# Performance work log

Measured on AMD Instinct MI355X. Metric: run time of the kernel, lower is better.

## Reference

```python
import jax, jax.numpy as jnp
import numpy as np

N_NODES = 50000
N_EDGES = 1200000
NODE_DIM = 64
HIDDEN = 64
OUT_DIM = 1
N_LAYERS = 3


def setup_inputs() -> dict:
    key = jax.random.key(0)
    ks = jax.random.split(key, 16)
    inp = {
        "H": jax.random.normal(ks[0], (N_NODES, NODE_DIM), dtype=jnp.float32),
        "edge_index": jax.random.randint(ks[1], (2, N_EDGES), 0, N_NODES, dtype=jnp.int64),
        "E": jax.random.normal(ks[2], (N_EDGES, 16), dtype=jnp.float32),
    }
    # per-layer params: node_encoder (enc) and update_w (upd); weights stored [in, out]
    for i in range(N_LAYERS):
        in_dim = NODE_DIM if i == 0 else HIDDEN
        s = 1.0 / np.sqrt(in_dim)
        inp[f"enc_w{i}"] = jax.random.uniform(ks[3 + 2 * i], (in_dim, HIDDEN), jnp.float32, -s, s)
        inp[f"enc_b{i}"] = jax.random.uniform(ks[4 + 2 * i], (HIDDEN,), jnp.float32, -s, s)
        sh = 1.0 / np.sqrt(HIDDEN)
        inp[f"upd_w{i}"] = jax.random.uniform(ks[9 + 2 * i], (HIDDEN, HIDDEN), jnp.float32, -sh, sh)
        inp[f"upd_b{i}"] = jax.random.uniform(ks[10 + 2 * i], (HIDDEN,), jnp.float32, -sh, sh)
    so = 1.0 / np.sqrt(HIDDEN)
    inp["out_w"] = jax.random.uniform(ks[15], (HIDDEN, OUT_DIM), jnp.float32, -so, so)
    inp["out_b"] = jnp.zeros((OUT_DIM,), jnp.float32)
    return inp


def _gcn_forward(H, edge_index, params):
    u, v = edge_index[0], edge_index[1]
    # symmetric normalization with implicit self-loop degree bump (calc_norm_factor)
    deg = jax.ops.segment_sum(jnp.ones(u.shape[0], H.dtype), u, num_segments=N_NODES) + 1.0
    dis = deg ** -0.5  # deg >= 1, never inf
    norm = dis[u] * dis[v]  # [n_edges]
    for i in range(N_LAYERS):
        enc_w, enc_b, upd_w, upd_b = params[i]
        H = H @ enc_w + enc_b                      # node_encoder
        msgs = norm[:, None] * H[u]                # gather + scale
        agg = jax.ops.segment_sum(msgs, v, num_segments=N_NODES)  # scatter-add
        H = jax.nn.relu((agg + H) @ upd_w + upd_b)  # update + ReLU (dropout = identity in eval)
    return H


def reference(H, edge_index, E, enc_w0, enc_b0, upd_w0, upd_b0, enc_w1, enc_b1,
              upd_w1, upd_b1, enc_w2, enc_b2, upd_w2, upd_b2, out_w, out_b):
    params = [(enc_w0, enc_b0, upd_w0, upd_b0),
              (enc_w1, enc_b1, upd_w1, upd_b1),
              (enc_w2, enc_b2, upd_w2, upd_b2)]
    Hf = _gcn_forward(H, edge_index, params)
    graph_emb = jnp.mean(Hf, axis=0, keepdims=True)  # [1, HIDDEN] readout (batch=None)
    return graph_emb @ out_w + out_b                 # [1, OUT_DIM]
```

## Files before the change

kernel.cpp:

```cpp
#include <hip/hip_runtime.h>
#include <hip/hip_fp16.h>

#define NN 50000
#define NE 1200000
#define DIM 64
#define NB 782
#define SLICES 512
#define ES 2344
#define VCAP 2048
#define GB 782
#define FRONT_LDS 33792
#define FB 3125

__device__ __forceinline__ void fold_body(char* smem, int i,
                                          const float* __restrict__ E,
                                          const float* __restrict__ e,
                                          const float* __restrict__ U,
                                          const float* __restrict__ ub,
                                          float* __restrict__ Wp,
                                          float* __restrict__ cvec,
                                          float* __restrict__ dvec) {
    float (*Es)[64] = (float(*)[64])smem;
    float (*Us)[64] = (float(*)[64])(smem + 16384);
    int t = threadIdx.x;
#pragma unroll
    for (int j = 0; j < 4; ++j) {
        int idx = t + j * 256;
        int r = idx >> 4, c = (idx & 15) << 2;
        *(float4*)&Es[r][c] = *(const float4*)&E[r * 64 + c];
        *(float4*)&Us[r][c] = *(const float4*)&U[r * 64 + c];
    }
    __syncthreads();
    int r0 = (t >> 4) * 4;
    int c0 = (t & 15) * 4;
    float acc[4][4] = {};
#pragma unroll
    for (int k = 0; k < 64; k += 4) {
        float4 b0 = *(float4*)&Us[k + 0][c0];
        float4 b1 = *(float4*)&Us[k + 1][c0];
        float4 b2 = *(float4*)&Us[k + 2][c0];
        float4 b3 = *(float4*)&Us[k + 3][c0];
#pragma unroll
        for (int q = 0; q < 4; ++q) {
            float4 av = *(float4*)&Es[r0 + q][k];
            acc[q][0] = fmaf(av.x, b0.x, fmaf(av.y, b1.x, fmaf(av.z, b2.x, fmaf(av.w, b3.x, acc[q][0]))));
            acc[q][1] = fmaf(av.x, b0.y, fmaf(av.y, b1.y, fmaf(av.z, b2.y, fmaf(av.w, b3.y, acc[q][1]))));
            acc[q][2] = fmaf(av.x, b0.z, fmaf(av.y, b1.z, fmaf(av.z, b2.z, fmaf(av.w, b3.z, acc[q][2]))));
            acc[q][3] = fmaf(av.x, b0.w, fmaf(av.y, b1.w, fmaf(av.z, b2.w, fmaf(av.w, b3.w, acc[q][3]))));
        }
    }
    float* W = Wp + i * 4096;
#pragma unroll
    for (int q = 0; q < 4; ++q)
        *(float4*)&W[(r0 + q) * 64 + c0] = make_float4(acc[q][0], acc[q][1], acc[q][2], acc[q][3]);
    if (t < 64) {
        float sc = 0.f;
        for (int k = 0; k < 64; ++k) sc = fmaf(e[k], Us[k][t], sc);
        cvec[i * 64 + t] = sc;
        dvec[i * 64 + t] = sc + ub[t];
    }
}


__device__ __forceinline__ void lsort_body(char* smem, const int* __restrict__ ei,
                                           ushort* __restrict__ usort,
                                           int* __restrict__ ebuf,
                                           int* __restrict__ lpart_u,
                                           int* __restrict__ lpart_v,
                                           int s) {
    int* hist = (int*)smem;
    int* wsum = (int*)(smem + 3136);
    ushort* sbu = (ushort*)(smem + 4160);
    int* sbv = (int*)(smem + 8848);
    int t = threadIdx.x;
    int w = t >> 6, l = t & 63;
    int e0 = s * ES, e1 = min(e0 + ES, NE), len = e1 - e0;
    int i0 = t * 4;

    int uv[10], vv[10];
#pragma unroll
    for (int j = 0; j < 10; ++j) {
        int e = e0 + t + j * 256;
        uv[j] = (e < e1) ? ei[e] : -1;
        vv[j] = (e < e1) ? ei[NE + e] : -1;
    }

    for (int i = t; i < NB; i += 256) hist[i] = 0;
    __syncthreads();
#pragma unroll
    for (int j = 0; j < 10; ++j)
        if (uv[j] >= 0) atomicAdd(&hist[uv[j] >> 6], 1);
    __syncthreads();
    {
        int h0 = (i0 + 0 < NB) ? hist[i0 + 0] : 0;
        int h1 = (i0 + 1 < NB) ? hist[i0 + 1] : 0;
        int h2 = (i0 + 2 < NB) ? hist[i0 + 2] : 0;
        int h3 = (i0 + 3 < NB) ? hist[i0 + 3] : 0;
        int p1 = h0, p2 = h0 + h1, p3 = p2 + h2, p4 = p3 + h3;
        int inc = p4;
        for (int o = 1; o < 64; o <<= 1) {
            int x = __shfl_up(inc, o, 64);
            if (l >= o) inc += x;
        }
        if (l == 63) wsum[w] = inc;
        __syncthreads();
        int base = 0;
#pragma unroll
        for (int j = 0; j < 4; ++j) if (j < w) base += wsum[j];
        int total = wsum[0] + wsum[1] + wsum[2] + wsum[3];
        int excl = base + inc - p4;
        int* lpu = lpart_u + s * (NB + 1);
        if (i0 + 0 < NB) { lpu[i0 + 0] = excl;      hist[i0 + 0] = excl; }
        if (i0 + 1 < NB) { lpu[i0 + 1] = excl + p1; hist[i0 + 1] = excl + p1; }
        if (i0 + 2 < NB) { lpu[i0 + 2] = excl + p2; hist[i0 + 2] = excl + p2; }
        if (i0 + 3 < NB) { lpu[i0 + 3] = excl + p3; hist[i0 + 3] = excl + p3; }
        if (t == 255) lpu[NB] = total;
    }
    __syncthreads();
#pragma unroll
    for (int j = 0; j < 10; ++j)
        if (uv[j] >= 0) {
            int pos = atomicAdd(&hist[uv[j] >> 6], 1);
            sbu[pos] = (ushort)uv[j];
        }
    __syncthreads();
    for (int i = t; i < len; i += 256) usort[e0 + i] = sbu[i];
    for (int i = t; i < NB; i += 256) hist[i] = 0;
    __syncthreads();

#pragma unroll
    for (int j = 0; j < 10; ++j)
        if (vv[j] >= 0) atomicAdd(&hist[vv[j] >> 6], 1);
    __syncthreads();
    {
        int h0 = (i0 + 0 < NB) ? hist[i0 + 0] : 0;
        int h1 = (i0 + 1 < NB) ? hist[i0 + 1] : 0;
        int h2 = (i0 + 2 < NB) ? hist[i0 + 2] : 0;
        int h3 = (i0 + 3 < NB) ? hist[i0 + 3] : 0;
        int p1 = h0, p2 = h0 + h1, p3 = p2 + h2, p4 = p3 + h3;
        int inc = p4;
        for (int o = 1; o < 64; o <<= 1) {
            int x = __shfl_up(inc, o, 64);
            if (l >= o) inc += x;
        }
        if (l == 63) wsum[w] = inc;
        __syncthreads();
        int base = 0;
#pragma unroll
        for (int j = 0; j < 4; ++j) if (j < w) base += wsum[j];
        int total = wsum[0] + wsum[1] + wsum[2] + wsum[3];
        int excl = base + inc - p4;
        int* lpv = lpart_v + s * (NB + 1);
        if (i0 + 0 < NB) { lpv[i0 + 0] = excl;      hist[i0 + 0] = excl; }
        if (i0 + 1 < NB) { lpv[i0 + 1] = excl + p1; hist[i0 + 1] = excl + p1; }
        if (i0 + 2 < NB) { lpv[i0 + 2] = excl + p2; hist[i0 + 2] = excl + p2; }
        if (i0 + 3 < NB) { lpv[i0 + 3] = excl + p3; hist[i0 + 3] = excl + p3; }
        if (t == 255) lpv[NB] = total;
    }
    __syncthreads();
#pragma unroll
    for (int j = 0; j < 10; ++j)
        if (vv[j] >= 0) {
            int pos = atomicAdd(&hist[vv[j] >> 6], 1);
            sbv[pos] = uv[j] | ((vv[j] & 63) << 16);
        }
    __syncthreads();
    for (int i = t; i < len; i += 256) ebuf[e0 + i] = sbv[i];
}

__device__ __forceinline__ void gemm0_body(char* smem, int blk,
                                           const float* __restrict__ H,
                                           const float* __restrict__ E0,
                                           const float* __restrict__ U0,
                                           __half* __restrict__ Ph) {
    float (*As)[68] = (float(*)[68])smem;
    float (*Bs)[64] = (float(*)[64])(smem + 17408);
    int t = threadIdx.x;
    int row0 = blk * 64;
#pragma unroll
    for (int i = 0; i < 4; ++i) {
        int idx = t + i * 256;
        int r = idx >> 4, c = (idx & 15) << 2;
        float4 val = make_float4(0.f, 0.f, 0.f, 0.f);
        if (row0 + r < NN) val = *(const float4*)&H[(size_t)(row0 + r) * DIM + c];
        *(float4*)&As[r][c] = val;
        *(float4*)&Bs[r][c] = *(const float4*)&E0[r * DIM + c];
    }
    __syncthreads();
    int r0 = (t >> 4) * 4;
    int c0 = (t & 15) * 4;
    float acc[4][4] = {};
#pragma unroll
    for (int k = 0; k < 64; k += 4) {
        float4 b0 = *(float4*)&Bs[k + 0][c0];
        float4 b1 = *(float4*)&Bs[k + 1][c0];
        float4 b2 = *(float4*)&Bs[k + 2][c0];
        float4 b3 = *(float4*)&Bs[k + 3][c0];
#pragma unroll
        for (int i = 0; i < 4; ++i) {
            float4 av = *(float4*)&As[r0 + i][k];
            acc[i][0] = fmaf(av.x, b0.x, fmaf(av.y, b1.x, fmaf(av.z, b2.x, fmaf(av.w, b3.x, acc[i][0]))));
            acc[i][1] = fmaf(av.x, b0.y, fmaf(av.y, b1.y, fmaf(av.z, b2.y, fmaf(av.w, b3.y, acc[i][1]))));
            acc[i][2] = fmaf(av.x, b0.z, fmaf(av.y, b1.z, fmaf(av.z, b2.z, fmaf(av.w, b3.z, acc[i][2]))));
            acc[i][3] = fmaf(av.x, b0.w, fmaf(av.y, b1.w, fmaf(av.z, b2.w, fmaf(av.w, b3.w, acc[i][3]))));
        }
    }
    __syncthreads();
#pragma unroll
    for (int i = 0; i < 4; ++i)
        *(float4*)&As[r0 + i][c0] = make_float4(acc[i][0], acc[i][1], acc[i][2], acc[i][3]);
#pragma unroll
    for (int i = 0; i < 4; ++i) {
        int idx = t + i * 256;
        int r = idx >> 4, c = (idx & 15) << 2;
        *(float4*)&Bs[r][c] = *(const float4*)&U0[r * DIM + c];
    }
    __syncthreads();
    float acc2[4][4] = {};
#pragma unroll
    for (int k = 0; k < 64; k += 4) {
        float4 b0 = *(float4*)&Bs[k + 0][c0];
        float4 b1 = *(float4*)&Bs[k + 1][c0];
        float4 b2 = *(float4*)&Bs[k + 2][c0];
        float4 b3 = *(float4*)&Bs[k + 3][c0];
#pragma unroll
        for (int i = 0; i < 4; ++i) {
            float4 av = *(float4*)&As[r0 + i][k];
            acc2[i][0] = fmaf(av.x, b0.x, fmaf(av.y, b1.x, fmaf(av.z, b2.x, fmaf(av.w, b3.x, acc2[i][0]))));
            acc2[i][1] = fmaf(av.x, b0.y, fmaf(av.y, b1.y, fmaf(av.z, b2.y, fmaf(av.w, b3.y, acc2[i][1]))));
            acc2[i][2] = fmaf(av.x, b0.z, fmaf(av.y, b1.z, fmaf(av.z, b2.z, fmaf(av.w, b3.z, acc2[i][2]))));
            acc2[i][3] = fmaf(av.x, b0.w, fmaf(av.y, b1.w, fmaf(av.z, b2.w, fmaf(av.w, b3.w, acc2[i][3]))));
        }
    }
#pragma unroll
    for (int i = 0; i < 4; ++i) {
        int r = row0 + r0 + i;
        if (r < NN) {
            __half2 p0 = __floats2half2_rn(acc2[i][0], acc2[i][1]);
            __half2 p1 = __floats2half2_rn(acc2[i][2], acc2[i][3]);
            uint2 pk;
            pk.x = *(unsigned int*)&p0;
            pk.y = *(unsigned int*)&p1;
            *(uint2*)&Ph[(size_t)r * DIM + c0] = pk;
        }
    }
}

__global__ __launch_bounds__(256, 2) void k_front(const int* __restrict__ ei,
                                                  ushort* __restrict__ usort,
                                                  int* __restrict__ ebuf,
                                                  int* __restrict__ lpart_u,
                                                  int* __restrict__ lpart_v,
                                                  const float* __restrict__ H,
                                                  const float* __restrict__ E0, const float* __restrict__ e0,
                                                  const float* __restrict__ U0, const float* __restrict__ ub0,
                                                  const float* __restrict__ E1, const float* __restrict__ e1,
                                                  const float* __restrict__ U1, const float* __restrict__ ub1,
                                                  const float* __restrict__ E2, const float* __restrict__ e2,
                                                  const float* __restrict__ U2, const float* __restrict__ ub2,
                                                  __half* __restrict__ Ph,
                                                  float* __restrict__ Wp,
                                                  float* __restrict__ cvec,
                                                  float* __restrict__ dvec) {
    extern __shared__ char smem[];
    int b = blockIdx.x;
    if (b < 256)
        lsort_body(smem, ei, usort, ebuf, lpart_u, lpart_v, b);
    else if (b < 512)
        gemm0_body(smem, b - 256, H, E0, U0, Ph);
    else if (b < 768)
        lsort_body(smem, ei, usort, ebuf, lpart_u, lpart_v, b - 256);
    else if (b < 512 + GB)
        gemm0_body(smem, b - 512, H, E0, U0, Ph);
    else {
        int i = b - (512 + GB);
        const float* E  = (i == 0) ? E0  : (i == 1) ? E1  : E2;
        const float* e  = (i == 0) ? e0  : (i == 1) ? e1  : e2;
        const float* U  = (i == 0) ? U0  : (i == 1) ? U1  : U2;
        const float* ub = (i == 0) ? ub0 : (i == 1) ? ub1 : ub2;
        fold_body(smem, i, E, e, U, ub, Wp, cvec, dvec);
    }
}

__global__ __launch_bounds__(256) void k_prep(const ushort* __restrict__ usort,
                                              const int* __restrict__ lpart_u,
                                              const int* __restrict__ ebuf,
                                              const int* __restrict__ lpart_v,
                                              float* __restrict__ dis,
                                              ushort* __restrict__ edges,
                                              int* __restrict__ row_ptr,
                                              float* __restrict__ colsum) {
    __shared__ int cache[VCAP];
    __shared__ int cnt[64];
    __shared__ int cur[64];
    __shared__ int wsum4[4];
    __shared__ int rsum4[4];
    __shared__ int sh[64];
    int bid = blockIdx.x;
    int t = threadIdx.x, w = t >> 6, l = t & 63;
    if (bid < NB) {
        int b = bid;
        if (b == 0 && t < 64) colsum[t] = 0.f;
        if (t < 64) sh[t] = 0;
        __syncthreads();
        for (int s = t; s < SLICES; s += 256) {
            const int* row = lpart_u + s * (NB + 1);
            int st = row[b], en = row[b + 1];
            for (int i = st; i < en; ++i)
                atomicAdd(&sh[usort[s * ES + i] & 63], 1);
        }
        __syncthreads();
        int n = (b << 6) + t;
        if (t < 64 && n < NN) dis[n] = rsqrtf((float)sh[t] + 1.0f);
        return;
    }
    int b = bid - NB;
    int s0 = t * 2, s1 = t * 2 + 1;
    const int* r0p = lpart_v + s0 * (NB + 1);
    const int* r1p = lpart_v + s1 * (NB + 1);
    int a0 = r0p[b], a1 = r0p[b + 1];
    int c0 = r1p[b], c1 = r1p[b + 1];
    int len0 = a1 - a0, len1 = c1 - c0;
    int tl = len0 + len1;
    int ts = a0 + c0;
    int inc = tl;
    for (int o = 1; o < 64; o <<= 1) {
        int x = __shfl_up(inc, o, 64);
        if (l >= o) inc += x;
    }
    int tss = ts;
    for (int off = 32; off; off >>= 1) tss += __shfl_down(tss, off, 64);
    if (l == 63) wsum4[w] = inc;
    if (l == 0) rsum4[w] = tss;
    if (t < 64) cnt[t] = 0;
    __syncthreads();
    int base = 0;
#pragma unroll
    for (int j = 0; j < 4; ++j) if (j < w) base += wsum4[j];
    int n = wsum4[0] + wsum4[1] + wsum4[2] + wsum4[3];
    int rbase = rsum4[0] + rsum4[1] + rsum4[2] + rsum4[3];
    int pos = base + inc - tl;
    if (n <= VCAP) {
        for (int i = 0; i < len0; ++i) cache[pos + i] = ebuf[s0 * ES + a0 + i];
        int pos1 = pos + len0;
        for (int i = 0; i < len1; ++i) cache[pos1 + i] = ebuf[s1 * ES + c0 + i];
        __syncthreads();
        for (int i = t; i < n; i += 256)
            atomicAdd(&cnt[(cache[i] >> 16) & 63], 1);
        __syncthreads();
        if (w == 0) {
            int c = cnt[l];
            int inc2 = c;
            for (int o = 1; o < 64; o <<= 1) {
                int x = __shfl_up(inc2, o, 64);
                if (l >= o) inc2 += x;
            }
            int excl = inc2 - c;
            cur[l] = rbase + excl;
            row_ptr[(b << 6) + l] = rbase + excl;
        }
        __syncthreads();
        for (int i = t; i < n; i += 256) {
            int rec = cache[i];
            int p2 = atomicAdd(&cur[(rec >> 16) & 63], 1);
            edges[p2] = (ushort)(rec & 0xFFFF);
        }
    } else {
        for (int s = t; s < SLICES; s += 256) {
            const int* row = lpart_v + s * (NB + 1);
            int st = row[b], en = row[b + 1];
            for (int i = st; i < en; ++i)
                atomicAdd(&cnt[(ebuf[s * ES + i] >> 16) & 63], 1);
        }
        __syncthreads();
        if (w == 0) {
            int c = cnt[l];
            int inc2 = c;
            for (int o = 1; o < 64; o <<= 1) {
                int x = __shfl_up(inc2, o, 64);
                if (l >= o) inc2 += x;
            }
            int excl = inc2 - c;
            cur[l] = rbase + excl;
            row_ptr[(b << 6) + l] = rbase + excl;
        }
        __syncthreads();
        for (int s = t; s < SLICES; s += 256) {
            const int* row = lpart_v + s * (NB + 1);
            int st = row[b], en = row[b + 1];
            for (int i = st; i < en; ++i) {
                int rec = ebuf[s * ES + i];
                int p2 = atomicAdd(&cur[(rec >> 16) & 63], 1);
                edges[p2] = (ushort)(rec & 0xFFFF);
            }
        }
    }
}

template<bool FIRST>
__device__ __forceinline__ void agg_node(const uint4* __restrict__ Pq4,
                                         const float* __restrict__ dis,
                                         const int* __restrict__ row_ptr,
                                         const ushort* __restrict__ edges,
                                         const float* __restrict__ cvec,
                                         const float* __restrict__ dvec,
                                         float* __restrict__ sarr,
                                         ushort* se, float* swt,
                                         int node, int l, int g, int p,
                                         float out[8]) {
    int start = row_ptr[node];
    int num = row_ptr[node + 1] - start;
    float4 a0 = {0.f, 0.f, 0.f, 0.f};
    float4 a1 = {0.f, 0.f, 0.f, 0.f};
    float sw = 0.f;
    for (int base = 0; base < num; base += 64) {
        int lim = min(64, num - base);
        ushort u = 0;
        float wv = 0.f;
        if (l < lim) { u = edges[start + base + l]; wv = dis[u]; }
        se[l] = u;
        swt[l] = wv;
        __builtin_amdgcn_wave_barrier();
        int octs = (lim + 7) >> 3;
        int rr[8]; float ww[8]; uint4 hh[8];
#pragma unroll
        for (int q = 0; q < 8; ++q)
            if (q < octs) { rr[q] = se[8 * q + g]; ww[q] = swt[8 * q + g]; }
#pragma unroll
        for (int q = 0; q < 8; ++q)
            if (q < octs) hh[q] = Pq4[(rr[q] << 3) + p];
#pragma unroll
        for (int q = 0; q < 8; ++q)
            if (q < octs) {
                float wt = ww[q];
                if (FIRST) sw += wt;
                float2 f0 = __half22float2(*(const __half2*)&hh[q].x);
                float2 f1 = __half22float2(*(const __half2*)&hh[q].y);
                float2 f2 = __half22float2(*(const __half2*)&hh[q].z);
                float2 f3 = __half22float2(*(const __half2*)&hh[q].w);
                a0.x = fmaf(wt, f0.x, a0.x);
                a0.y = fmaf(wt, f0.y, a0.y);
                a0.z = fmaf(wt, f1.x, a0.z);
                a0.w = fmaf(wt, f1.y, a0.w);
                a1.x = fmaf(wt, f2.x, a1.x);
                a1.y = fmaf(wt, f2.y, a1.y);
                a1.z = fmaf(wt, f3.x, a1.z);
                a1.w = fmaf(wt, f3.y, a1.w);
            }
        __builtin_amdgcn_wave_barrier();
    }
#pragma unroll
    for (int m = 8; m < 64; m <<= 1) {
        a0.x += __shfl_xor(a0.x, m, 64);
        a0.y += __shfl_xor(a0.y, m, 64);
        a0.z += __shfl_xor(a0.z, m, 64);
        a0.w += __shfl_xor(a0.w, m, 64);
        a1.x += __shfl_xor(a1.x, m, 64);
        a1.y += __shfl_xor(a1.y, m, 64);
        a1.z += __shfl_xor(a1.z, m, 64);
        a1.w += __shfl_xor(a1.w, m, 64);
        if (FIRST) sw += __shfl_xor(sw, m, 64);
    }
    if (g == 0) {
        float dv = dis[node];
        float sv;
        if (FIRST) {
            sv = dv * sw;
            if (p == 0) sarr[node] = sv;
        } else {
            sv = sarr[node];
        }
        uint4 pv = Pq4[(node << 3) + p];
        float2 s0 = __half22float2(*(const __half2*)&pv.x);
        float2 s1 = __half22float2(*(const __half2*)&pv.y);
        float2 s2 = __half22float2(*(const __half2*)&pv.z);
        float2 s3 = __half22float2(*(const __half2*)&pv.w);
        float4 cA = *(const float4*)&cvec[p << 3];
        float4 cB = *(const float4*)&cvec[(p << 3) + 4];
        float4 dA = *(const float4*)&dvec[p << 3];
        float4 dB = *(const float4*)&dvec[(p << 3) + 4];
        out[0] = fmaxf(fmaf(dv, a0.x, s0.x) + fmaf(sv, cA.x, dA.x), 0.f);
        out[1] = fmaxf(fmaf(dv, a0.y, s0.y) + fmaf(sv, cA.y, dA.y), 0.f);
        out[2] = fmaxf(fmaf(dv, a0.z, s1.x) + fmaf(sv, cA.z, dA.z), 0.f);
        out[3] = fmaxf(fmaf(dv, a0.w, s1.y) + fmaf(sv, cA.w, dA.w), 0.f);
        out[4] = fmaxf(fmaf(dv, a1.x, s2.x) + fmaf(sv, cB.x, dB.x), 0.f);
        out[5] = fmaxf(fmaf(dv, a1.y, s2.y) + fmaf(sv, cB.y, dB.y), 0.f);
        out[6] = fmaxf(fmaf(dv, a1.z, s3.x) + fmaf(sv, cB.z, dB.z), 0.f);
        out[7] = fmaxf(fmaf(dv, a1.w, s3.y) + fmaf(sv, cB.w, dB.w), 0.f);
    }
}

template<bool FIRST>
__global__ __launch_bounds__(256) void k_agggemm(const uint4* __restrict__ Pq4,
                                                 const float* __restrict__ dis,
                                                 const int* __restrict__ row_ptr,
                                                 const ushort* __restrict__ edges,
                                                 const float* __restrict__ cvec,
                                                 const float* __restrict__ dvec,
                                                 float* __restrict__ sarr,
                                                 const float* __restrict__ W,
                                                 __half* __restrict__ Phout) {
    __shared__ float As[16][68];
    __shared__ float Bs[64][64];
    __shared__ ushort se[4][64];
    __shared__ float swt[4][64];
    int t = threadIdx.x, w = t >> 6, l = t & 63;
    int g = l >> 3, p = l & 7;
    int node0 = blockIdx.x << 4;
#pragma unroll
    for (int i = 0; i < 4; ++i) {
        int idx = t + i * 256;
        int r = idx >> 4, c = (idx & 15) << 2;
        *(float4*)&Bs[r][c] = *(const float4*)&W[r * 64 + c];
    }
#pragma unroll 1
    for (int nn = 0; nn < 4; ++nn) {
        int node = node0 + (w << 2) + nn;
        float out[8];
        agg_node<FIRST>(Pq4, dis, row_ptr, edges, cvec, dvec, sarr,
                        se[w], swt[w], node, l, g, p, out);
        if (g == 0) {
            int r = (w << 2) + nn;
            *(float4*)&As[r][p << 3] = make_float4(out[0], out[1], out[2], out[3]);
            *(float4*)&As[r][(p << 3) + 4] = make_float4(out[4], out[5], out[6], out[7]);
        }
    }
    __syncthreads();
    int r = t >> 4;
    int c0 = (t & 15) << 2;
    float acc0 = 0.f, acc1 = 0.f, acc2 = 0.f, acc3 = 0.f;
#pragma unroll
    for (int k = 0; k < 64; k += 4) {
        float4 b0 = *(float4*)&Bs[k + 0][c0];
        float4 b1 = *(float4*)&Bs[k + 1][c0];
        float4 b2 = *(float4*)&Bs[k + 2][c0];
        float4 b3 = *(float4*)&Bs[k + 3][c0];
        float4 av = *(float4*)&As[r][k];
        acc0 = fmaf(av.x, b0.x, fmaf(av.y, b1.x, fmaf(av.z, b2.x, fmaf(av.w, b3.x, acc0))));
        acc1 = fmaf(av.x, b0.y, fmaf(av.y, b1.y, fmaf(av.z, b2.y, fmaf(av.w, b3.y, acc1))));
        acc2 = fmaf(av.x, b0.z, fmaf(av.y, b1.z, fmaf(av.z, b2.z, fmaf(av.w, b3.z, acc2))));
        acc3 = fmaf(av.x, b0.w, fmaf(av.y, b1.w, fmaf(av.z, b2.w, fmaf(av.w, b3.w, acc3))));
    }
    __half2 h0 = __floats2half2_rn(acc0, acc1);
    __half2 h1 = __floats2half2_rn(acc2, acc3);
    uint2 pk;
    pk.x = *(unsigned int*)&h0;
    pk.y = *(unsigned int*)&h1;
    *(uint2*)&Phout[(size_t)(node0 + r) * DIM + c0] = pk;
}

__global__ __launch_bounds__(256) void k_agg3(const uint4* __restrict__ Pq4,
                                              const float* __restrict__ dis,
                                              const int* __restrict__ row_ptr,
                                              const ushort* __restrict__ edges,
                                              const float* __restrict__ cvec,
                                              const float* __restrict__ dvec,
                                              float* __restrict__ sarr,
                                              __half* __restrict__ Hh) {
    __shared__ ushort se[4][64];
    __shared__ float swt[4][64];
    int t = threadIdx.x, w = t >> 6, l = t & 63;
    int g = l >> 3, p = l & 7;
    int node = (blockIdx.x << 2) + w;
    float out[8];
    agg_node<false>(Pq4, dis, row_ptr, edges, cvec, dvec, sarr,
                    se[w], swt[w], node, l, g, p, out);
    if (g == 0) {
        __half2 h0 = __floats2half2_rn(out[0], out[1]);
        __half2 h1 = __floats2half2_rn(out[2], out[3]);
        __half2 h2 = __floats2half2_rn(out[4], out[5]);
        __half2 h3 = __floats2half2_rn(out[6], out[7]);
        uint4 pk;
        pk.x = *(unsigned int*)&h0;
        pk.y = *(unsigned int*)&h1;
        pk.z = *(unsigned int*)&h2;
        pk.w = *(unsigned int*)&h3;
        *(uint4*)&Hh[((size_t)node << 6) + (p << 3)] = pk;
    }
}

__global__ __launch_bounds__(256) void k_colsum(const __half* __restrict__ Hh,
                                                float* __restrict__ colsum) {
    __shared__ float scs[64];
    int t = threadIdx.x;
    if (t < 64) scs[t] = 0.f;
    __syncthreads();
    int p = t & 7;
    float a[8] = {};
    for (int r = blockIdx.x * 32 + (t >> 3); r < NN; r += 256 * 32) {
        uint4 hv = *(const uint4*)&Hh[((size_t)r << 6) + (p << 3)];
        float2 f0 = __half22float2(*(const __half2*)&hv.x);
        float2 f1 = __half22float2(*(const __half2*)&hv.y);
        float2 f2 = __half22float2(*(const __half2*)&hv.z);
        float2 f3 = __half22float2(*(const __half2*)&hv.w);
        a[0] += f0.x; a[1] += f0.y; a[2] += f1.x; a[3] += f1.y;
        a[4] += f2.x; a[5] += f2.y; a[6] += f3.x; a[7] += f3.y;
    }
#pragma unroll
    for (int j = 0; j < 8; ++j) atomicAdd(&scs[(p << 3) + j], a[j]);
    __syncthreads();
    if (t < 64) atomicAdd(&colsum[t], scs[t]);
}

__global__ void k_out(const float* __restrict__ colsum, const float* __restrict__ out_w,
                      const float* __restrict__ out_b, float* __restrict__ out) {
    int f = threadIdx.x;
    float v = colsum[f] * (1.0f / (float)NN) * out_w[f];
    for (int off = 32; off; off >>= 1) v += __shfl_down(v, off, 64);
    if (f == 0) out[0] = v + out_b[0];
}

extern "C" void kernel_launch(void* const* d_in, const int* in_sizes, int n_in,
                              void* d_out, int out_size, void* d_ws, size_t ws_size,
                              hipStream_t stream) {
    const float* H  = (const float*)d_in[0];
    const int*   ei = (const int*)d_in[1];
    const float* enc_w[3] = { (const float*)d_in[3], (const float*)d_in[7],  (const float*)d_in[11] };
    const float* enc_b[3] = { (const float*)d_in[4], (const float*)d_in[8],  (const float*)d_in[12] };
    const float* upd_w[3] = { (const float*)d_in[5], (const float*)d_in[9],  (const float*)d_in[13] };
    const float* upd_b[3] = { (const float*)d_in[6], (const float*)d_in[10], (const float*)d_in[14] };
    const float* out_w = (const float*)d_in[15];
    const float* out_b = (const float*)d_in[16];
    float* out = (float*)d_out;

    size_t off = 0;
    auto carve = [&](size_t bytes) {
        void* p = (char*)d_ws + off;
        off = (off + bytes + 255) & ~(size_t)255;
        return p;
    };
    int*    lpart_u = (int*)carve((size_t)SLICES * (NB + 1) * 4);
    int*    lpart_v = (int*)carve((size_t)SLICES * (NB + 1) * 4);
    float*  dis     = (float*)carve((size_t)NN * 4);
    float*  sarr    = (float*)carve((size_t)NN * 4);
    ushort* usort   = (ushort*)carve((size_t)SLICES * ES * 2);
    int*    ebuf    = (int*)carve((size_t)SLICES * ES * 4);
    ushort* edges   = (ushort*)carve((size_t)NE * 2);
    int*    row_ptr = (int*)carve((size_t)(NN + 65) * 4);
    __half* PhA     = (__half*)carve((size_t)NN * DIM * 2);
    __half* PhB     = (__half*)carve((size_t)NN * DIM * 2);
    __half* Hh      = (__half*)carve((size_t)NN * DIM * 2);
    float*  Wp      = (float*)carve(3 * 64 * 64 * 4);
    float*  cvec    = (float*)carve(3 * 64 * 4);
    float*  dvec    = (float*)carve(3 * 64 * 4);
    float*  colsum  = (float*)carve(64 * 4);

    const uint4* PqA = (const uint4*)PhA;
    const uint4* PqB = (const uint4*)PhB;

    k_front<<<512 + GB + 3, 256, FRONT_LDS, stream>>>(ei, usort, ebuf, lpart_u, lpart_v, H,
                                                      enc_w[0], enc_b[0], upd_w[0], upd_b[0],
                                                      enc_w[1], enc_b[1], upd_w[1], upd_b[1],
                                                      enc_w[2], enc_b[2], upd_w[2], upd_b[2],
                                                      PhA, Wp, cvec, dvec);
    k_prep<<<2 * NB, 256, 0, stream>>>(usort, lpart_u, ebuf, lpart_v,
                                       dis, edges, row_ptr, colsum);

    k_agggemm<true><<<FB, 256, 0, stream>>>(PqA, dis, row_ptr, edges,
                                            cvec + 0, dvec + 0, sarr, Wp + 4096, PhB);
    k_agggemm<false><<<FB, 256, 0, stream>>>(PqB, dis, row_ptr, edges,
                                             cvec + 64, dvec + 64, sarr, Wp + 8192, PhA);
    k_agg3<<<NN / 4, 256, 0, stream>>>(PqA, dis, row_ptr, edges,
                                       cvec + 128, dvec + 128, sarr, Hh);

    k_colsum<<<256, 256, 0, stream>>>(Hh, colsum);
    k_out<<<1, 64, 0, stream>>>(colsum, out_w, out_b, out);
}
```

Measured before the change: 316.4 us.

## Fuse last-layer aggregation with column-sum readout and per-wave GEMM rows

Merges the third-layer aggregation kernel with the column-sum readout, so the final node features are never written to a half-precision buffer and read back. Each wave now accumulates column sums over its 4 nodes and combines them through shared-memory atomics. Inside the aggregation, the per-edge degree-scale staging in LDS is replaced by direct gathers of dis after the feature loads, and the self-row load is hoisted to the start. The agg+GEMM kernel swaps the block-wide barrier for a wave barrier, since each wave only multiplies its own rows. This saves a launch and a full-size intermediate buffer, at the cost of more global gathers of dis and different floating-point summation order.

```diff
diff --git a/kernel.cpp b/kernel.cpp
--- a/kernel.cpp
+++ b/kernel.cpp
@@ -405,30 +405,30 @@
                                          const float* __restrict__ cvec,
                                          const float* __restrict__ dvec,
                                          float* __restrict__ sarr,
-                                         ushort* se, float* swt,
+                                         ushort* se,
                                          int node, int l, int g, int p,
                                          float out[8]) {
     int start = row_ptr[node];
     int num = row_ptr[node + 1] - start;
+    uint4 pv = Pq4[(node << 3) + p];
     float4 a0 = {0.f, 0.f, 0.f, 0.f};
     float4 a1 = {0.f, 0.f, 0.f, 0.f};
     float sw = 0.f;
     for (int base = 0; base < num; base += 64) {
         int lim = min(64, num - base);
-        ushort u = 0;
-        float wv = 0.f;
-        if (l < lim) { u = edges[start + base + l]; wv = dis[u]; }
-        se[l] = u;
-        swt[l] = wv;
+        se[l] = (l < lim) ? edges[start + base + l] : 0;
         __builtin_amdgcn_wave_barrier();
         int octs = (lim + 7) >> 3;
         int rr[8]; float ww[8]; uint4 hh[8];
 #pragma unroll
         for (int q = 0; q < 8; ++q)
-            if (q < octs) { rr[q] = se[8 * q + g]; ww[q] = swt[8 * q + g]; }
+            if (q < octs) rr[q] = se[8 * q + g];
 #pragma unroll
         for (int q = 0; q < 8; ++q)
             if (q < octs) hh[q] = Pq4[(rr[q] << 3) + p];
+#pragma unroll
+        for (int q = 0; q < 8; ++q)
+            if (q < octs) ww[q] = (8 * q + g < lim) ? dis[rr[q]] : 0.f;
 #pragma unroll
         for (int q = 0; q < 8; ++q)
             if (q < octs) {
@@ -470,7 +470,6 @@
         } else {
             sv = sarr[node];
         }
-        uint4 pv = Pq4[(node << 3) + p];
         float2 s0 = __half22float2(*(const __half2*)&pv.x);
         float2 s1 = __half22float2(*(const __half2*)&pv.y);
         float2 s2 = __half22float2(*(const __half2*)&pv.z);
@@ -503,7 +502,6 @@
     __shared__ float As[16][68];
     __shared__ float Bs[64][64];
     __shared__ ushort se[4][64];
-    __shared__ float swt[4][64];
     int t = threadIdx.x, w = t >> 6, l = t & 63;
     int g = l >> 3, p = l & 7;
     int node0 = blockIdx.x << 4;
@@ -513,21 +511,22 @@
         int r = idx >> 4, c = (idx & 15) << 2;
         *(float4*)&Bs[r][c] = *(const float4*)&W[r * 64 + c];
     }
+    __syncthreads();
 #pragma unroll 1
     for (int nn = 0; nn < 4; ++nn) {
         int node = node0 + (w << 2) + nn;
         float out[8];
         agg_node<FIRST>(Pq4, dis, row_ptr, edges, cvec, dvec, sarr,
-                        se[w], swt[w], node, l, g, p, out);
+                        se[w], node, l, g, p, out);
         if (g == 0) {
             int r = (w << 2) + nn;
             *(float4*)&As[r][p << 3] = make_float4(out[0], out[1], out[2], out[3]);
             *(float4*)&As[r][(p << 3) + 4] = make_float4(out[4], out[5], out[6], out[7]);
         }
     }
-    __syncthreads();
-    int r = t >> 4;
-    int c0 = (t & 15) << 2;
+    __builtin_amdgcn_wave_barrier();
+    int r = (w << 2) + (l >> 4);
+    int c0 = (l & 15) << 2;
     float acc0 = 0.f, acc1 = 0.f, acc2 = 0.f, acc3 = 0.f;
 #pragma unroll
     for (int k = 0; k < 64; k += 4) {
@@ -549,55 +548,37 @@
     *(uint2*)&Phout[(size_t)(node0 + r) * DIM + c0] = pk;
 }
 
-__global__ __launch_bounds__(256) void k_agg3(const uint4* __restrict__ Pq4,
-                                              const float* __restrict__ dis,
-                                              const int* __restrict__ row_ptr,
-                                              const ushort* __restrict__ edges,
-                                              const float* __restrict__ cvec,
-                                              const float* __restrict__ dvec,
-                                              float* __restrict__ sarr,
-                                              __half* __restrict__ Hh) {
+__global__ __launch_bounds__(256) void k_aggsum(const uint4* __restrict__ Pq4,
+                                                const float* __restrict__ dis,
+                                                const int* __restrict__ row_ptr,
+                                                const ushort* __restrict__ edges,
+                                                const float* __restrict__ cvec,
+                                                const float* __restrict__ dvec,
+                                                float* __restrict__ sarr,
+                                                float* __restrict__ colsum) {
     __shared__ ushort se[4][64];
-    __shared__ float swt[4][64];
+    __shared__ float scs[64];
     int t = threadIdx.x, w = t >> 6, l = t & 63;
     int g = l >> 3, p = l & 7;
-    int node = (blockIdx.x << 2) + w;
-    float out[8];
-    agg_node<false>(Pq4, dis, row_ptr, edges, cvec, dvec, sarr,
-                    se[w], swt[w], node, l, g, p, out);
+    if (t < 64) scs[t] = 0.f;
+    __syncthreads();
+    int node0 = blockIdx.x << 4;
+    float cs[8] = {};
+#pragma unroll 1
+    for (int nn = 0; nn < 4; ++nn) {
+        int node = node0 + (w << 2) + nn;
+        float out[8];
+        agg_node<false>(Pq4, dis, row_ptr, edges, cvec, dvec, sarr,
+                        se[w], node, l, g, p, out);
+        if (g == 0) {
+#pragma unroll
+            for (int j = 0; j < 8; ++j) cs[j] += out[j];
+        }
+    }
     if (g == 0) {
-        __half2 h0 = __floats2half2_rn(out[0], out[1]);
-        __half2 h1 = __floats2half2_rn(out[2], out[3]);
-        __half2 h2 = __floats2half2_rn(out[4], out[5]);
-        __half2 h3 = __floats2half2_rn(out[6], out[7]);
-        uint4 pk;
-        pk.x = *(unsigned int*)&h0;
-        pk.y = *(unsigned int*)&h1;
-        pk.z = *(unsigned int*)&h2;
-        pk.w = *(unsigned int*)&h3;
-        *(uint4*)&Hh[((size_t)node << 6) + (p << 3)] = pk;
-    }
-}
-
-__global__ __launch_bounds__(256) void k_colsum(const __half* __restrict__ Hh,
-                                                float* __restrict__ colsum) {
-    __shared__ float scs[64];
-    int t = threadIdx.x;
-    if (t < 64) scs[t] = 0.f;
-    __syncthreads();
-    int p = t & 7;
-    float a[8] = {};
-    for (int r = blockIdx.x * 32 + (t >> 3); r < NN; r += 256 * 32) {
-        uint4 hv = *(const uint4*)&Hh[((size_t)r << 6) + (p << 3)];
-        float2 f0 = __half22float2(*(const __half2*)&hv.x);
-        float2 f1 = __half22float2(*(const __half2*)&hv.y);
-        float2 f2 = __half22float2(*(const __half2*)&hv.z);
-        float2 f3 = __half22float2(*(const __half2*)&hv.w);
-        a[0] += f0.x; a[1] += f0.y; a[2] += f1.x; a[3] += f1.y;
-        a[4] += f2.x; a[5] += f2.y; a[6] += f3.x; a[7] += f3.y;
-    }
-#pragma unroll
-    for (int j = 0; j < 8; ++j) atomicAdd(&scs[(p << 3) + j], a[j]);
+#pragma unroll
+        for (int j = 0; j < 8; ++j) atomicAdd(&scs[(p << 3) + j], cs[j]);
+    }
     __syncthreads();
     if (t < 64) atomicAdd(&colsum[t], scs[t]);
 }
@@ -639,7 +620,6 @@
     int*    row_ptr = (int*)carve((size_t)(NN + 65) * 4);
     __half* PhA     = (__half*)carve((size_t)NN * DIM * 2);
     __half* PhB     = (__half*)carve((size_t)NN * DIM * 2);
-    __half* Hh      = (__half*)carve((size_t)NN * DIM * 2);
     float*  Wp      = (float*)carve(3 * 64 * 64 * 4);
     float*  cvec    = (float*)carve(3 * 64 * 4);
     float*  dvec    = (float*)carve(3 * 64 * 4);
@@ -660,9 +640,8 @@
                                             cvec + 0, dvec + 0, sarr, Wp + 4096, PhB);
     k_agggemm<false><<<FB, 256, 0, stream>>>(PqB, dis, row_ptr, edges,
                                              cvec + 64, dvec + 64, sarr, Wp + 8192, PhA);
-    k_agg3<<<NN / 4, 256, 0, stream>>>(PqA, dis, row_ptr, edges,
-                                       cvec + 128, dvec + 128, sarr, Hh);
-
-    k_colsum<<<256, 256, 0, stream>>>(Hh, colsum);
+    k_aggsum<<<FB, 256, 0, stream>>>(PqA, dis, row_ptr, edges,
+                                     cvec + 128, dvec + 128, sarr, colsum);
+
     k_out<<<1, 64, 0, stream>>>(colsum, out_w, out_b, out);
 }
```

New measurement: 362.0 us. +14.4%, slower.

## Halve nodes per agg-GEMM block, make GEMM wave-local, load dis after gathers

Applied to the files above, without the earlier changes.

Each k_agggemm block now handles 8 nodes instead of 16, so twice as many blocks launch. Each wave does its own 2-row slice of the 64x64 GEMM after a wave barrier rather than a block-wide __syncthreads. The per-edge dis weights are now loaded per lane after the feature gathers are issued, which removes the shared-memory weight staging. The self row load is hoisted to the start of the node loop so it overlaps the aggregation. This targets the block-wide sync stall and low parallelism, at the cost of reloading the weight matrix W into LDS twice as often and issuing more scattered dis loads.

```diff
diff --git a/kernel.cpp b/kernel.cpp
--- a/kernel.cpp
+++ b/kernel.cpp
@@ -10,7 +10,7 @@
 #define VCAP 2048
 #define GB 782
 #define FRONT_LDS 33792
-#define FB 3125
+#define AGB 6250
 
 __device__ __forceinline__ void fold_body(char* smem, int i,
                                           const float* __restrict__ E,
@@ -405,30 +405,30 @@
                                          const float* __restrict__ cvec,
                                          const float* __restrict__ dvec,
                                          float* __restrict__ sarr,
-                                         ushort* se, float* swt,
+                                         ushort* se,
                                          int node, int l, int g, int p,
                                          float out[8]) {
     int start = row_ptr[node];
     int num = row_ptr[node + 1] - start;
+    uint4 pv = Pq4[(node << 3) + p];
     float4 a0 = {0.f, 0.f, 0.f, 0.f};
     float4 a1 = {0.f, 0.f, 0.f, 0.f};
     float sw = 0.f;
     for (int base = 0; base < num; base += 64) {
         int lim = min(64, num - base);
-        ushort u = 0;
-        float wv = 0.f;
-        if (l < lim) { u = edges[start + base + l]; wv = dis[u]; }
-        se[l] = u;
-        swt[l] = wv;
+        se[l] = (l < lim) ? edges[start + base + l] : 0;
         __builtin_amdgcn_wave_barrier();
         int octs = (lim + 7) >> 3;
         int rr[8]; float ww[8]; uint4 hh[8];
 #pragma unroll
         for (int q = 0; q < 8; ++q)
-            if (q < octs) { rr[q] = se[8 * q + g]; ww[q] = swt[8 * q + g]; }
+            if (q < octs) rr[q] = se[8 * q + g];
 #pragma unroll
         for (int q = 0; q < 8; ++q)
             if (q < octs) hh[q] = Pq4[(rr[q] << 3) + p];
+#pragma unroll
+        for (int q = 0; q < 8; ++q)
+            if (q < octs) ww[q] = (8 * q + g < lim) ? dis[rr[q]] : 0.f;
 #pragma unroll
         for (int q = 0; q < 8; ++q)
             if (q < octs) {
@@ -470,7 +470,6 @@
         } else {
             sv = sarr[node];
         }
-        uint4 pv = Pq4[(node << 3) + p];
         float2 s0 = __half22float2(*(const __half2*)&pv.x);
         float2 s1 = __half22float2(*(const __half2*)&pv.y);
         float2 s2 = __half22float2(*(const __half2*)&pv.z);
@@ -500,53 +499,47 @@
                                                  float* __restrict__ sarr,
                                                  const float* __restrict__ W,
                                                  __half* __restrict__ Phout) {
-    __shared__ float As[16][68];
+    __shared__ float As[8][68];
     __shared__ float Bs[64][64];
     __shared__ ushort se[4][64];
-    __shared__ float swt[4][64];
     int t = threadIdx.x, w = t >> 6, l = t & 63;
     int g = l >> 3, p = l & 7;
-    int node0 = blockIdx.x << 4;
+    int node0 = blockIdx.x << 3;
 #pragma unroll
     for (int i = 0; i < 4; ++i) {
         int idx = t + i * 256;
         int r = idx >> 4, c = (idx & 15) << 2;
         *(float4*)&Bs[r][c] = *(const float4*)&W[r * 64 + c];
     }
+    __syncthreads();
 #pragma unroll 1
-    for (int nn = 0; nn < 4; ++nn) {
-        int node = node0 + (w << 2) + nn;
+    for (int nn = 0; nn < 2; ++nn) {
+        int node = node0 + (w << 1) + nn;
         float out[8];
         agg_node<FIRST>(Pq4, dis, row_ptr, edges, cvec, dvec, sarr,
-                        se[w], swt[w], node, l, g, p, out);
+                        se[w], node, l, g, p, out);
         if (g == 0) {
-            int r = (w << 2) + nn;
+            int r = (w << 1) + nn;
             *(float4*)&As[r][p << 3] = make_float4(out[0], out[1], out[2], out[3]);
             *(float4*)&As[r][(p << 3) + 4] = make_float4(out[4], out[5], out[6], out[7]);
         }
     }
-    __syncthreads();
-    int r = t >> 4;
-    int c0 = (t & 15) << 2;
-    float acc0 = 0.f, acc1 = 0.f, acc2 = 0.f, acc3 = 0.f;
+    __builtin_amdgcn_wave_barrier();
+    int r = (w << 1) + (l >> 5);
+    int c0 = (l & 31) << 1;
+    float acc0 = 0.f, acc1 = 0.f;
 #pragma unroll
     for (int k = 0; k < 64; k += 4) {
-        float4 b0 = *(float4*)&Bs[k + 0][c0];
-        float4 b1 = *(float4*)&Bs[k + 1][c0];
-        float4 b2 = *(float4*)&Bs[k + 2][c0];
-        float4 b3 = *(float4*)&Bs[k + 3][c0];
+        float2 b0 = *(float2*)&Bs[k + 0][c0];
+        float2 b1 = *(float2*)&Bs[k + 1][c0];
+        float2 b2 = *(float2*)&Bs[k + 2][c0];
+        float2 b3 = *(float2*)&Bs[k + 3][c0];
         float4 av = *(float4*)&As[r][k];
         acc0 = fmaf(av.x, b0.x, fmaf(av.y, b1.x, fmaf(av.z, b2.x, fmaf(av.w, b3.x, acc0))));
         acc1 = fmaf(av.x, b0.y, fmaf(av.y, b1.y, fmaf(av.z, b2.y, fmaf(av.w, b3.y, acc1))));
-        acc2 = fmaf(av.x, b0.z, fmaf(av.y, b1.z, fmaf(av.z, b2.z, fmaf(av.w, b3.z, acc2))));
-        acc3 = fmaf(av.x, b0.w, fmaf(av.y, b1.w, fmaf(av.z, b2.w, fmaf(av.w, b3.w, acc3))));
     }
     __half2 h0 = __floats2half2_rn(acc0, acc1);
-    __half2 h1 = __floats2half2_rn(acc2, acc3);
-    uint2 pk;
-    pk.x = *(unsigned int*)&h0;
-    pk.y = *(unsigned int*)&h1;
-    *(uint2*)&Phout[(size_t)(node0 + r) * DIM + c0] = pk;
+    *(unsigned int*)&Phout[(size_t)(node0 + r) * DIM + c0] = *(unsigned int*)&h0;
 }
 
 __global__ __launch_bounds__(256) void k_agg3(const uint4* __restrict__ Pq4,
@@ -558,13 +551,12 @@
                                               float* __restrict__ sarr,
                                               __half* __restrict__ Hh) {
     __shared__ ushort se[4][64];
-    __shared__ float swt[4][64];
     int t = threadIdx.x, w = t >> 6, l = t & 63;
     int g = l >> 3, p = l & 7;
     int node = (blockIdx.x << 2) + w;
     float out[8];
     agg_node<false>(Pq4, dis, row_ptr, edges, cvec, dvec, sarr,
-                    se[w], swt[w], node, l, g, p, out);
+                    se[w], node, l, g, p, out);
     if (g == 0) {
         __half2 h0 = __floats2half2_rn(out[0], out[1]);
         __half2 h1 = __floats2half2_rn(out[2], out[3]);
@@ -656,13 +648,12 @@
     k_prep<<<2 * NB, 256, 0, stream>>>(usort, lpart_u, ebuf, lpart_v,
                                        dis, edges, row_ptr, colsum);
 
-    k_agggemm<true><<<FB, 256, 0, stream>>>(PqA, dis, row_ptr, edges,
-                                            cvec + 0, dvec + 0, sarr, Wp + 4096, PhB);
-    k_agggemm<false><<<FB, 256, 0, stream>>>(PqB, dis, row_ptr, edges,
-                                             cvec + 64, dvec + 64, sarr, Wp + 8192, PhA);
+    k_agggemm<true><<<AGB, 256, 0, stream>>>(PqA, dis, row_ptr, edges,
+                                             cvec + 0, dvec + 0, sarr, Wp + 4096, PhB);
+    k_agggemm<false><<<AGB, 256, 0, stream>>>(PqB, dis, row_ptr, edges,
+                                              cvec + 64, dvec + 64, sarr, Wp + 8192, PhA);
     k_agg3<<<NN / 4, 256, 0, stream>>>(PqA, dis, row_ptr, edges,
                                        cvec + 128, dvec + 128, sarr, Hh);
-
     k_colsum<<<256, 256, 0, stream>>>(Hh, colsum);
     k_out<<<1, 64, 0, stream>>>(colsum, out_w, out_b, out);
 }
```

Measured after the change: 324.6 us. +2.6%, slower.
